# Kernel optimization log

Hardware: AMD Instinct MI355X
Metric: run time of the kernel (lower is better)

Reference implementation:

```python
import jax, jax.numpy as jnp
import numpy as np

B, N, NODE_DIM, HID, HEAD = 32, 1024, 14, 64, 128
EDGE_PROB = 0.01


def setup_inputs() -> dict:
    key = jax.random.key(0)
    ks = jax.random.split(key, 12)
    x = jax.random.normal(ks[0], (B, N, NODE_DIM), dtype=jnp.float32)
    # sparse binary adjacency with self-loops (matches eye + edge scatter)
    adj = (jax.random.uniform(ks[1], (B, N, N)) < EDGE_PROB).astype(jnp.float32)
    adjacency = jnp.maximum(adj, jnp.eye(N, dtype=jnp.float32)[None])
    def lin(k, din, dout):
        kw, kb = jax.random.split(k)
        w = jax.random.normal(kw, (din, dout), dtype=jnp.float32) / np.sqrt(din)
        b = jnp.zeros((dout,), dtype=jnp.float32)
        return w, b
    W1, b1 = lin(ks[2], NODE_DIM, HID)
    W2, b2 = lin(ks[3], HID, HID)
    W3, b3 = lin(ks[4], HID, HID)
    Wf1, bf1 = lin(ks[5], HID, HEAD)
    Wf2, bf2 = lin(ks[6], HEAD, 1)
    return {"x": x, "adjacency": adjacency, "W1": W1, "b1": b1, "W2": W2,
            "b2": b2, "W3": W3, "b3": b3, "Wf1": Wf1, "bf1": bf1,
            "Wf2": Wf2, "bf2": bf2}


def _dense_graph_conv(x, norm_adj, W, b):
    # (D^-1/2 A D^-1/2) @ x, then linear
    return jnp.einsum('bnm,bmd->bnd', norm_adj, x) @ W + b


def reference(x, adjacency, W1, b1, W2, b2, W3, b3, Wf1, bf1, Wf2, bf2):
    degree = adjacency.sum(axis=-1)                      # [B,N]
    d_inv_sqrt = jnp.clip(degree, 1.0, None) ** -0.5
    norm_adj = d_inv_sqrt[..., :, None] * adjacency * d_inv_sqrt[..., None, :]
    h = jax.nn.relu(_dense_graph_conv(x, norm_adj, W1, b1))
    h = jax.nn.relu(_dense_graph_conv(h, norm_adj, W2, b2))
    h = jax.nn.relu(_dense_graph_conv(h, norm_adj, W3, b3))
    pooled = h.mean(axis=1)                              # [B,HID]
    return jax.nn.relu(pooled @ Wf1 + bf1) @ Wf2 + bf2   # [B,1]
```

## Files before the change

### kernel.cpp

```cpp
#include <hip/hip_runtime.h>
#include <math.h>

#define NN 1024
#define HID 64
#define HEADD 128
#define NODE_DIM 14
#define BATCH 32
#define CAP 64
#define ROWS (BATCH * NN)
#define RPW 8

__device__ __forceinline__ int swz4(int blk, int wv) {
    int x = blk & 7, q = blk >> 3;
    int batch = x + 8 * (q >> 8);
    return batch * NN + ((q & 255) << 2) + wv;
}
__device__ __forceinline__ int swz32(int blk, int wv) {
    int x = blk & 7, q = blk >> 3;
    int batch = x + 8 * (q >> 5);
    return batch * NN + ((q & 31) << 5) + wv * RPW;
}

__global__ __launch_bounds__(256) void k_build(const float* __restrict__ adj,
                                               const float* __restrict__ x,
                                               const float* __restrict__ W1,
                                               int* __restrict__ csr,
                                               int* __restrict__ nnz_g,
                                               float* __restrict__ dinv,
                                               float* __restrict__ g1,
                                               float* __restrict__ pooled) {
    __shared__ float sW1[NODE_DIM * HID];
    for (int i = threadIdx.x; i < NODE_DIM * HID; i += 256) sW1[i] = W1[i];
    if (blockIdx.x < 8) pooled[blockIdx.x * 256 + threadIdx.x] = 0.f;
    int wv = threadIdx.x >> 6, lane = threadIdx.x & 63;
    int row = swz4(blockIdx.x, wv);
    const float4* rp = reinterpret_cast<const float4*>(adj + (size_t)row * NN);
    unsigned long long lt = ((unsigned long long)1 << lane) - 1;
    int base = 0;
#pragma unroll
    for (int j = 0; j < 4; ++j) {
        float4 v = rp[lane + 64 * j];
        float vv[4] = {v.x, v.y, v.z, v.w};
#pragma unroll
        for (int k = 0; k < 4; ++k) {
            unsigned long long mk = __ballot(vv[k] != 0.0f);
            if (vv[k] != 0.0f) {
                int pos = base + __popcll(mk & lt);
                if (pos < CAP) csr[row * CAP + pos] = (lane + 64 * j) * 4 + k;
            }
            base += __popcll(mk);
        }
    }
    if (lane == 0) {
        nnz_g[row] = base < CAP ? base : CAP;
        dinv[row] = 1.0f / sqrtf((float)(base < 1 ? 1 : base));
    }
    __syncthreads();
    float acc = 0.f;
    const float* xr = x + (size_t)row * NODE_DIM;
#pragma unroll
    for (int d = 0; d < NODE_DIM; ++d) acc += xr[d] * sW1[d * HID + lane];
    g1[(size_t)row * HID + lane] = acc;
}

__device__ __forceinline__ float spmm_row(const float* __restrict__ g_in,
                                          int bbase, int n, int idx, float dv,
                                          int lane) {
    float acc = 0.f;
    int k = 0;
    for (; k + 8 <= n; k += 8) {
        int j[8]; float w[8], v[8];
#pragma unroll
        for (int u = 0; u < 8; ++u) { j[u] = __shfl(idx, k + u); w[u] = __shfl(dv, k + u); }
#pragma unroll
        for (int u = 0; u < 8; ++u) v[u] = g_in[(size_t)(bbase + j[u]) * HID + lane];
#pragma unroll
        for (int u = 0; u < 8; ++u) acc += w[u] * v[u];
    }
    for (; k + 4 <= n; k += 4) {
        int j[4]; float w[4], v[4];
#pragma unroll
        for (int u = 0; u < 4; ++u) { j[u] = __shfl(idx, k + u); w[u] = __shfl(dv, k + u); }
#pragma unroll
        for (int u = 0; u < 4; ++u) v[u] = g_in[(size_t)(bbase + j[u]) * HID + lane];
#pragma unroll
        for (int u = 0; u < 4; ++u) acc += w[u] * v[u];
    }
    for (; k < n; ++k)
        acc += __shfl(dv, k) * g_in[(size_t)(bbase + __shfl(idx, k)) * HID + lane];
    return acc;
}

__global__ __launch_bounds__(256) void k_layer1(const float* __restrict__ g_in,
                                                const int* __restrict__ csr,
                                                const int* __restrict__ nnz_g,
                                                const float* __restrict__ dinv,
                                                const float* __restrict__ bias,
                                                const float* __restrict__ W,
                                                float* __restrict__ g_out,
                                                int2* __restrict__ edge) {
    __shared__ float sW[HID * HID];
    for (int i = threadIdx.x; i < HID * HID; i += 256) sW[i] = W[i];
    int wv = threadIdx.x >> 6, lane = threadIdx.x & 63;
    int row0 = swz32(blockIdx.x, wv);
    int bbase = row0 & ~(NN - 1);
    float bb = bias[lane];
    float h[RPW], o[RPW];
#pragma unroll
    for (int r = 0; r < RPW; ++r) {
        int row = row0 + r;
        int n = nnz_g[row];
        int idx = (lane < n) ? csr[row * CAP + lane] : 0;
        float dv = (lane < n) ? dinv[bbase + idx] : 0.f;
        if (lane < n) edge[row * CAP + lane] = make_int2(idx, __float_as_int(dv));
        h[r] = fmaxf(dinv[row] * spmm_row(g_in, bbase, n, idx, dv, lane) + bb, 0.f);
        o[r] = 0.f;
    }
    __syncthreads();
    for (int d = 0; d < HID; ++d) {
        float w = sW[d * HID + lane];
#pragma unroll
        for (int r = 0; r < RPW; ++r) o[r] += __shfl(h[r], d) * w;
    }
#pragma unroll
    for (int r = 0; r < RPW; ++r)
        g_out[(size_t)(row0 + r) * HID + lane] = o[r];
}

__global__ __launch_bounds__(256) void k_layer2(const float* __restrict__ g_in,
                                                const int2* __restrict__ edge,
                                                const int* __restrict__ nnz_g,
                                                const float* __restrict__ dinv,
                                                const float* __restrict__ bias,
                                                const float* __restrict__ W,
                                                float* __restrict__ g_out) {
    __shared__ float sW[HID * HID];
    for (int i = threadIdx.x; i < HID * HID; i += 256) sW[i] = W[i];
    int wv = threadIdx.x >> 6, lane = threadIdx.x & 63;
    int row0 = swz32(blockIdx.x, wv);
    int bbase = row0 & ~(NN - 1);
    float bb = bias[lane];
    float h[RPW], o[RPW];
#pragma unroll
    for (int r = 0; r < RPW; ++r) {
        int row = row0 + r;
        int n = nnz_g[row];
        int2 e = (lane < n) ? edge[row * CAP + lane] : make_int2(0, 0);
        float dv = __int_as_float(e.y);
        h[r] = fmaxf(dinv[row] * spmm_row(g_in, bbase, n, e.x, dv, lane) + bb, 0.f);
        o[r] = 0.f;
    }
    __syncthreads();
    for (int d = 0; d < HID; ++d) {
        float w = sW[d * HID + lane];
#pragma unroll
        for (int r = 0; r < RPW; ++r) o[r] += __shfl(h[r], d) * w;
    }
#pragma unroll
    for (int r = 0; r < RPW; ++r)
        g_out[(size_t)(row0 + r) * HID + lane] = o[r];
}

__global__ __launch_bounds__(256) void k_layer3(const float* __restrict__ g_in,
                                                const int2* __restrict__ edge,
                                                const int* __restrict__ nnz_g,
                                                const float* __restrict__ dinv,
                                                const float* __restrict__ bias,
                                                float* __restrict__ pooled) {
    __shared__ float sred[4][HID];
    int wv = threadIdx.x >> 6, lane = threadIdx.x & 63;
    int row0 = swz32(blockIdx.x, wv);
    int bbase = row0 & ~(NN - 1);
    float bb = bias[lane];
    float s = 0.f;
#pragma unroll
    for (int r = 0; r < RPW; ++r) {
        int row = row0 + r;
        int n = nnz_g[row];
        int2 e = (lane < n) ? edge[row * CAP + lane] : make_int2(0, 0);
        float dv = __int_as_float(e.y);
        s += fmaxf(dinv[row] * spmm_row(g_in, bbase, n, e.x, dv, lane) + bb, 0.f);
    }
    sred[wv][lane] = s;
    __syncthreads();
    if (wv == 0) {
        float tot = sred[0][lane] + sred[1][lane] + sred[2][lane] + sred[3][lane];
        atomicAdd(&pooled[(bbase >> 10) * HID + lane], tot);
    }
}

__global__ __launch_bounds__(128) void k_head(const float* __restrict__ pooled_sum,
                                              const float* __restrict__ Wf1,
                                              const float* __restrict__ bf1,
                                              const float* __restrict__ Wf2,
                                              const float* __restrict__ bf2,
                                              float* __restrict__ out) {
    int b = blockIdx.x, t = threadIdx.x;
    __shared__ float p[HID];
    __shared__ float hid[HEADD];
    if (t < HID) p[t] = pooled_sum[b * HID + t] * (1.0f / NN);
    __syncthreads();
    float acc = bf1[t];
    for (int d = 0; d < HID; ++d) acc += p[d] * Wf1[d * HEADD + t];
    hid[t] = fmaxf(acc, 0.f);
    __syncthreads();
    if (t < 64) {
        float v = hid[t] * Wf2[t] + hid[t + 64] * Wf2[t + 64];
#pragma unroll
        for (int off = 32; off > 0; off >>= 1) v += __shfl_down(v, off, 64);
        if (t == 0) out[b] = v + bf2[0];
    }
}

extern "C" void kernel_launch(void* const* d_in, const int* in_sizes, int n_in,
                              void* d_out, int out_size, void* d_ws, size_t ws_size,
                              hipStream_t stream) {
    const float* x   = (const float*)d_in[0];
    const float* adj = (const float*)d_in[1];
    const float* W1  = (const float*)d_in[2];
    const float* b1  = (const float*)d_in[3];
    const float* W2  = (const float*)d_in[4];
    const float* b2  = (const float*)d_in[5];
    const float* W3  = (const float*)d_in[6];
    const float* b3  = (const float*)d_in[7];
    const float* Wf1 = (const float*)d_in[8];
    const float* bf1 = (const float*)d_in[9];
    const float* Wf2 = (const float*)d_in[10];
    const float* bf2 = (const float*)d_in[11];
    float* out = (float*)d_out;

    char* ws = (char*)d_ws;
    size_t off = 0;
    int*   csr    = (int*)(ws + off);  off += (size_t)ROWS * CAP * 4;
    int2*  edge   = (int2*)(ws + off); off += (size_t)ROWS * CAP * 8;
    int*   nnz_g  = (int*)(ws + off);  off += (size_t)ROWS * 4;
    float* dinv   = (float*)(ws + off); off += (size_t)ROWS * 4;
    float* pooled = (float*)(ws + off); off += 4096 * 4;
    float* g1     = (float*)(ws + off); off += (size_t)ROWS * HID * 4;
    float* g2     = (float*)(ws + off); off += (size_t)ROWS * HID * 4;
    float* g3     = (float*)(ws + off);

    k_build <<<ROWS / 4, 256, 0, stream>>>(adj, x, W1, csr, nnz_g, dinv, g1, pooled);
    k_layer1<<<ROWS / 32, 256, 0, stream>>>(g1, csr, nnz_g, dinv, b1, W2, g2, edge);
    k_layer2<<<ROWS / 32, 256, 0, stream>>>(g2, edge, nnz_g, dinv, b2, W3, g3);
    k_layer3<<<ROWS / 32, 256, 0, stream>>>(g3, edge, nnz_g, dinv, b3, pooled);
    k_head  <<<BATCH, 128, 0, stream>>>(pooled, Wf1, bf1, Wf2, bf2, out);
}
```

Before: 331.2 us.

## Use readlane broadcasts and register-resident weights in GCN layer kernels

Replaces __shfl broadcasts (ds_bpermute through LDS hardware) with v_readlane scalar broadcasts in the sparse gather and in the per-row 64x64 GEMM. Each lane now keeps its column of W in 64 registers instead of staging W in shared memory, which removes the __syncthreads and the LDS reads. The neighbor count is made wave-uniform with readfirstlane, the 8-wide gather unroll is dropped, and launch bounds request 4 blocks per CU. The trade-off is much higher register pressure and less memory-level parallelism in the gather loop.

```diff
diff --git a/kernel.cpp b/kernel.cpp
--- a/kernel.cpp
+++ b/kernel.cpp
@@ -19,6 +19,10 @@
     int x = blk & 7, q = blk >> 3;
     int batch = x + 8 * (q >> 5);
     return batch * NN + ((q & 31) << 5) + wv * RPW;
+}
+
+__device__ __forceinline__ float rl_f(float v, int k) {
+    return __int_as_float(__builtin_amdgcn_readlane(__float_as_int(v), k));
 }
 
 __global__ __launch_bounds__(256) void k_build(const float* __restrict__ adj,
@@ -68,105 +72,106 @@
                                           int lane) {
     float acc = 0.f;
     int k = 0;
-    for (; k + 8 <= n; k += 8) {
-        int j[8]; float w[8], v[8];
-#pragma unroll
-        for (int u = 0; u < 8; ++u) { j[u] = __shfl(idx, k + u); w[u] = __shfl(dv, k + u); }
-#pragma unroll
-        for (int u = 0; u < 8; ++u) v[u] = g_in[(size_t)(bbase + j[u]) * HID + lane];
-#pragma unroll
-        for (int u = 0; u < 8; ++u) acc += w[u] * v[u];
-    }
     for (; k + 4 <= n; k += 4) {
-        int j[4]; float w[4], v[4];
-#pragma unroll
-        for (int u = 0; u < 4; ++u) { j[u] = __shfl(idx, k + u); w[u] = __shfl(dv, k + u); }
-#pragma unroll
-        for (int u = 0; u < 4; ++u) v[u] = g_in[(size_t)(bbase + j[u]) * HID + lane];
-#pragma unroll
-        for (int u = 0; u < 4; ++u) acc += w[u] * v[u];
-    }
-    for (; k < n; ++k)
-        acc += __shfl(dv, k) * g_in[(size_t)(bbase + __shfl(idx, k)) * HID + lane];
+        int j0 = __builtin_amdgcn_readlane(idx, k);
+        int j1 = __builtin_amdgcn_readlane(idx, k + 1);
+        int j2 = __builtin_amdgcn_readlane(idx, k + 2);
+        int j3 = __builtin_amdgcn_readlane(idx, k + 3);
+        float w0 = rl_f(dv, k),     w1 = rl_f(dv, k + 1);
+        float w2 = rl_f(dv, k + 2), w3 = rl_f(dv, k + 3);
+        float v0 = g_in[(size_t)(bbase + j0) * HID + lane];
+        float v1 = g_in[(size_t)(bbase + j1) * HID + lane];
+        float v2 = g_in[(size_t)(bbase + j2) * HID + lane];
+        float v3 = g_in[(size_t)(bbase + j3) * HID + lane];
+        acc += w0 * v0; acc += w1 * v1; acc += w2 * v2; acc += w3 * v3;
+    }
+    for (; k < n; ++k) {
+        int j = __builtin_amdgcn_readlane(idx, k);
+        acc += rl_f(dv, k) * g_in[(size_t)(bbase + j) * HID + lane];
+    }
     return acc;
 }
 
-__global__ __launch_bounds__(256) void k_layer1(const float* __restrict__ g_in,
-                                                const int* __restrict__ csr,
-                                                const int* __restrict__ nnz_g,
-                                                const float* __restrict__ dinv,
-                                                const float* __restrict__ bias,
-                                                const float* __restrict__ W,
-                                                float* __restrict__ g_out,
-                                                int2* __restrict__ edge) {
-    __shared__ float sW[HID * HID];
-    for (int i = threadIdx.x; i < HID * HID; i += 256) sW[i] = W[i];
-    int wv = threadIdx.x >> 6, lane = threadIdx.x & 63;
+__device__ __forceinline__ void gemm_rows(const float h[RPW], const float wreg[HID],
+                                          float o[RPW]) {
+#pragma unroll
+    for (int r = 0; r < RPW; ++r) o[r] = 0.f;
+#pragma unroll
+    for (int d = 0; d < HID; ++d) {
+        float w = wreg[d];
+#pragma unroll
+        for (int r = 0; r < RPW; ++r) o[r] += rl_f(h[r], d) * w;
+    }
+}
+
+__global__ __launch_bounds__(256, 4) void k_layer1(const float* __restrict__ g_in,
+                                                   const int* __restrict__ csr,
+                                                   const int* __restrict__ nnz_g,
+                                                   const float* __restrict__ dinv,
+                                                   const float* __restrict__ bias,
+                                                   const float* __restrict__ W,
+                                                   float* __restrict__ g_out,
+                                                   int2* __restrict__ edge) {
+    int wv = threadIdx.x >> 6, lane = threadIdx.x & 63;
+    float wreg[HID];
+#pragma unroll
+    for (int d = 0; d < HID; ++d) wreg[d] = W[d * HID + lane];
     int row0 = swz32(blockIdx.x, wv);
     int bbase = row0 & ~(NN - 1);
     float bb = bias[lane];
-    float h[RPW], o[RPW];
+    float h[RPW];
 #pragma unroll
     for (int r = 0; r < RPW; ++r) {
         int row = row0 + r;
-        int n = nnz_g[row];
+        int n = __builtin_amdgcn_readfirstlane(nnz_g[row]);
         int idx = (lane < n) ? csr[row * CAP + lane] : 0;
         float dv = (lane < n) ? dinv[bbase + idx] : 0.f;
         if (lane < n) edge[row * CAP + lane] = make_int2(idx, __float_as_int(dv));
         h[r] = fmaxf(dinv[row] * spmm_row(g_in, bbase, n, idx, dv, lane) + bb, 0.f);
-        o[r] = 0.f;
-    }
-    __syncthreads();
-    for (int d = 0; d < HID; ++d) {
-        float w = sW[d * HID + lane];
-#pragma unroll
-        for (int r = 0; r < RPW; ++r) o[r] += __shfl(h[r], d) * w;
-    }
+    }
+    float o[RPW];
+    gemm_rows(h, wreg, o);
 #pragma unroll
     for (int r = 0; r < RPW; ++r)
         g_out[(size_t)(row0 + r) * HID + lane] = o[r];
 }
 
-__global__ __launch_bounds__(256) void k_layer2(const float* __restrict__ g_in,
-                                                const int2* __restrict__ edge,
-                                                const int* __restrict__ nnz_g,
-                                                const float* __restrict__ dinv,
-                                                const float* __restrict__ bias,
-                                                const float* __restrict__ W,
-                                                float* __restrict__ g_out) {
-    __shared__ float sW[HID * HID];
-    for (int i = threadIdx.x; i < HID * HID; i += 256) sW[i] = W[i];
-    int wv = threadIdx.x >> 6, lane = threadIdx.x & 63;
+__global__ __launch_bounds__(256, 4) void k_layer2(const float* __restrict__ g_in,
+                                                   const int2* __restrict__ edge,
+                                                   const int* __restrict__ nnz_g,
+                                                   const float* __restrict__ dinv,
+                                                   const float* __restrict__ bias,
+                                                   const float* __restrict__ W,
+                                                   float* __restrict__ g_out) {
+    int wv = threadIdx.x >> 6, lane = threadIdx.x & 63;
+    float wreg[HID];
+#pragma unroll
+    for (int d = 0; d < HID; ++d) wreg[d] = W[d * HID + lane];
     int row0 = swz32(blockIdx.x, wv);
     int bbase = row0 & ~(NN - 1);
     float bb = bias[lane];
-    float h[RPW], o[RPW];
+    float h[RPW];
 #pragma unroll
     for (int r = 0; r < RPW; ++r) {
         int row = row0 + r;
-        int n = nnz_g[row];
+        int n = __builtin_amdgcn_readfirstlane(nnz_g[row]);
         int2 e = (lane < n) ? edge[row * CAP + lane] : make_int2(0, 0);
         float dv = __int_as_float(e.y);
         h[r] = fmaxf(dinv[row] * spmm_row(g_in, bbase, n, e.x, dv, lane) + bb, 0.f);
-        o[r] = 0.f;
-    }
-    __syncthreads();
-    for (int d = 0; d < HID; ++d) {
-        float w = sW[d * HID + lane];
-#pragma unroll
-        for (int r = 0; r < RPW; ++r) o[r] += __shfl(h[r], d) * w;
-    }
+    }
+    float o[RPW];
+    gemm_rows(h, wreg, o);
 #pragma unroll
     for (int r = 0; r < RPW; ++r)
         g_out[(size_t)(row0 + r) * HID + lane] = o[r];
 }
 
-__global__ __launch_bounds__(256) void k_layer3(const float* __restrict__ g_in,
-                                                const int2* __restrict__ edge,
-                                                const int* __restrict__ nnz_g,
-                                                const float* __restrict__ dinv,
-                                                const float* __restrict__ bias,
-                                                float* __restrict__ pooled) {
+__global__ __launch_bounds__(256, 4) void k_layer3(const float* __restrict__ g_in,
+                                                   const int2* __restrict__ edge,
+                                                   const int* __restrict__ nnz_g,
+                                                   const float* __restrict__ dinv,
+                                                   const float* __restrict__ bias,
+                                                   float* __restrict__ pooled) {
     __shared__ float sred[4][HID];
     int wv = threadIdx.x >> 6, lane = threadIdx.x & 63;
     int row0 = swz32(blockIdx.x, wv);
@@ -176,7 +181,7 @@
 #pragma unroll
     for (int r = 0; r < RPW; ++r) {
         int row = row0 + r;
-        int n = nnz_g[row];
+        int n = __builtin_amdgcn_readfirstlane(nnz_g[row]);
         int2 e = (lane < n) ? edge[row * CAP + lane] : make_int2(0, 0);
         float dv = __int_as_float(e.y);
         s += fmaxf(dinv[row] * spmm_row(g_in, bbase, n, e.x, dv, lane) + bb, 0.f);
@@ -231,9 +236,9 @@
 
     char* ws = (char*)d_ws;
     size_t off = 0;
-    int*   csr    = (int*)(ws + off);  off += (size_t)ROWS * CAP * 4;
-    int2*  edge   = (int2*)(ws + off); off += (size_t)ROWS * CAP * 8;
-    int*   nnz_g  = (int*)(ws + off);  off += (size_t)ROWS * 4;
+    int*   csr    = (int*)(ws + off);   off += (size_t)ROWS * CAP * 4;
+    int2*  edge   = (int2*)(ws + off);  off += (size_t)ROWS * CAP * 8;
+    int*   nnz_g  = (int*)(ws + off);   off += (size_t)ROWS * 4;
     float* dinv   = (float*)(ws + off); off += (size_t)ROWS * 4;
     float* pooled = (float*)(ws + off); off += 4096 * 4;
     float* g1     = (float*)(ws + off); off += (size_t)ROWS * HID * 4;
```

Result: faster. 301.4 us (-9.0%).
